# Kernel tuning notes

Hardware: AMD Instinct MI355X
Metric: run time of the kernel (lower is better)

## Reference

```python
import jax, jax.numpy as jnp
import numpy as np

N = 50000      # nodes
E = 400000     # edges per hop
IN = 256       # in_channels
H = 4          # heads
C = 64         # out_channels per head
NEG = 0.2      # leaky relu negative slope


def setup_inputs() -> dict:
    key = jax.random.key(0)
    ks = jax.random.split(key, 10)
    x = jax.random.normal(ks[0], (N, IN), dtype=jnp.float32)
    edge_index1 = jax.random.randint(ks[1], (2, E), 0, N, dtype=jnp.int32)
    edge_index2 = jax.random.randint(ks[2], (2, E), 0, N, dtype=jnp.int32)
    s = 0.05
    Wl0 = jax.random.normal(ks[3], (IN, H * C), dtype=jnp.float32) * s
    Wr0 = jax.random.normal(ks[4], (IN, H * C), dtype=jnp.float32) * s
    att0 = jax.random.normal(ks[5], (H, C), dtype=jnp.float32) * s
    Wl1 = jax.random.normal(ks[6], (IN, H * C), dtype=jnp.float32) * s
    Wr1 = jax.random.normal(ks[7], (IN, H * C), dtype=jnp.float32) * s
    att1 = jax.random.normal(ks[8], (H, C), dtype=jnp.float32) * s
    return {"x": x, "Wl0": Wl0, "Wr0": Wr0, "att0": att0,
            "Wl1": Wl1, "Wr1": Wr1, "att1": att1,
            "edge_index1": edge_index1, "edge_index2": edge_index2}


def _gatv2_hop(x, Wl, Wr, att, src, dst):
    """One GATv2Conv hop (bias=False, residual=False, eval-mode dropout, concat=False)."""
    n = x.shape[0]
    xl = (x @ Wl).reshape(n, H, C)   # source-side projection
    xr = (x @ Wr).reshape(n, H, C)   # target-side projection
    # edge-wise GATv2 score: a^T leaky_relu(x_l[j] + x_r[i])
    m = jax.nn.leaky_relu(xl[src] + xr[dst], NEG)            # [E, H, C]
    e = jnp.einsum('ehc,hc->eh', m, att)                     # [E, H]
    # segment softmax over incoming edges of each destination node
    e_max = jax.lax.stop_gradient(
        jax.ops.segment_max(e, dst, num_segments=n))         # [N, H]
    ex = jnp.exp(e - e_max[dst])
    denom = jax.ops.segment_sum(ex, dst, num_segments=n)     # [N, H]
    alpha = ex / (denom[dst] + 1e-16)                        # [E, H]
    msg = xl[src] * alpha[:, :, None]                        # [E, H, C]
    out = jax.ops.segment_sum(msg, dst, num_segments=n)      # [N, H, C]
    return out.mean(axis=1)                                  # concat=False -> mean heads


def reference(x, Wl0, Wr0, att0, Wl1, Wr1, att1, edge_index1, edge_index2):
    n = x.shape[0]
    # hop 0: add_self_loops=True
    loop = jnp.arange(n, dtype=edge_index1.dtype)
    src0 = jnp.concatenate([edge_index1[0], loop])
    dst0 = jnp.concatenate([edge_index1[1], loop])
    out = _gatv2_hop(x, Wl0, Wr0, att0, src0, dst0)
    # hop 1: no self loops, scaled by 1/(k+1) = 1/2
    out = out + _gatv2_hop(x, Wl1, Wr1, att1, edge_index2[0], edge_index2[1]) / 2.0
    return out
```

## Files before the change

### kernel.cpp

```cpp
#include <hip/hip_runtime.h>

typedef unsigned int uint;
typedef unsigned short ushort;

typedef __bf16 bf16x8 __attribute__((ext_vector_type(8)));
typedef float f32x4 __attribute__((ext_vector_type(4)));
typedef float f32x2 __attribute__((ext_vector_type(2)));

#define CAP 48
#define RSTR 136

__device__ __forceinline__ float bf2f(ushort u) {
    return __uint_as_float(((uint)u) << 16);
}
__device__ __forceinline__ ushort f2bf(float f) {
    uint u = __float_as_uint(f);
    u += 0x7fffu + ((u >> 16) & 1u);
    return (ushort)(u >> 16);
}
__device__ __forceinline__ void load_lds16(const ushort* g, ushort* l) {
    __builtin_amdgcn_global_load_lds(
        (const __attribute__((address_space(1))) void*)g,
        (__attribute__((address_space(3))) void*)l, 16, 0, 0);
}
__device__ __forceinline__ f32x2 up2(uint u) {
    f32x2 r;
    r.x = __uint_as_float(u << 16);
    r.y = __uint_as_float(u & 0xffff0000u);
    return r;
}

template<int CTRL>
__device__ __forceinline__ float dppadd(float p) {
    int t = __builtin_amdgcn_update_dpp(0, __float_as_int(p), CTRL, 0xf, 0xf, true);
    return p + __int_as_float(t);
}

__global__ __launch_bounds__(256) void prep_scatter(
    const float* __restrict__ X, ushort* __restrict__ Xb, int Nrows, int Mpad,
    const float* __restrict__ Wl0, const float* __restrict__ Wr0,
    const float* __restrict__ Wl1, const float* __restrict__ Wr1,
    ushort* __restrict__ Wt,
    const int* __restrict__ ei1, const int* __restrict__ ei2,
    int* __restrict__ cnt0, int* __restrict__ srcs0,
    int* __restrict__ cnt1, int* __restrict__ srcs1,
    int E1, int E2, int SB)
{
    int blk = blockIdx.x;
    if (blk < SB) {
        int e = blk * 256 + threadIdx.x;
        if (e < E1) {
            int d = ei1[E1 + e];
            int pos = atomicAdd(&cnt0[d], 1);
            if (pos < CAP) srcs0[(size_t)d * CAP + pos] = ei1[e];
        } else if (e < E1 + E2) {
            int e2 = e - E1;
            int d = ei2[E2 + e2];
            int pos = atomicAdd(&cnt1[d], 1);
            if (pos < CAP) srcs1[(size_t)d * CAP + pos] = ei2[e2];
        }
        return;
    }
    blk -= SB;
    const int BX = Mpad / 8;
    if (blk < BX) {
        int i = blk * 256 + threadIdx.x;
        int base = i * 8;
        int row = base >> 8;
        ushort o[8];
        if (row < Nrows) {
            float4 v0 = *(const float4*)(X + base);
            float4 v1 = *(const float4*)(X + base + 4);
            o[0] = f2bf(v0.x); o[1] = f2bf(v0.y); o[2] = f2bf(v0.z); o[3] = f2bf(v0.w);
            o[4] = f2bf(v1.x); o[5] = f2bf(v1.y); o[6] = f2bf(v1.z); o[7] = f2bf(v1.w);
        } else {
#pragma unroll
            for (int j = 0; j < 8; j++) o[j] = 0;
        }
        *(uint4*)(Xb + base) = *(const uint4*)o;
        return;
    }
    blk -= BX;
    int n = blk;
    int k = threadIdx.x;
    const float* W = (n < 256) ? Wl0 : (n < 512) ? Wr0 : (n < 768) ? Wl1 : Wr1;
    Wt[n * 256 + k] = f2bf(W[k * 256 + (n & 255)]);
}

__global__ __launch_bounds__(256, 4) void gemm_mfma(
    const ushort* __restrict__ Xb,
    const ushort* __restrict__ Wt,
    ushort* __restrict__ XP,
    int Nrows, int Pp, int nbshift)
{
    int b = blockIdx.x;
    int xcd = b & 7;
    int i = b >> 3;
    int p = xcd * Pp + (i >> nbshift);
    int j = i & ((1 << nbshift) - 1);
    const int m0 = p * 128;
    const int n0g = j * 128;

    __shared__ ushort SH[2 * 128 * 64];
    ushort* As = SH;
    ushort* Bs = SH + 128 * 64;

    const int tid = threadIdx.x;
    const int w = tid >> 6, l = tid & 63;
    const int wm = w & 1, wn = w >> 1;

    f32x4 acc[4][4];
#pragma unroll
    for (int ii = 0; ii < 4; ii++)
#pragma unroll
        for (int jj = 0; jj < 4; jj++) acc[ii][jj] = (f32x4)(0.f);

    const int fr = l & 15, fq = l >> 4;
    int a_off[2][4], b_off[2][4];
#pragma unroll
    for (int g = 0; g < 2; g++)
#pragma unroll
        for (int t = 0; t < 4; t++) {
            int c = g * 4 + fq;
            int rA = wm * 64 + t * 16 + fr;
            a_off[g][t] = (rA * 8 + ((c + rA) & 7)) * 8;
            int rB = wn * 64 + t * 16 + fr;
            b_off[g][t] = (rB * 8 + ((c + rB) & 7)) * 8;
        }

    for (int k0 = 0; k0 < 256; k0 += 64) {
        __syncthreads();
#pragma unroll
        for (int rnd = 0; rnd < 4; rnd++) {
            int slot = rnd * 256 + tid;
            int row = slot >> 3;
            int c = ((slot & 7) - row) & 7;
            load_lds16(Xb + (size_t)(m0 + row) * 256 + k0 + c * 8,
                       &As[(rnd * 256 + w * 64) * 8]);
            load_lds16(Wt + (size_t)(n0g + row) * 256 + k0 + c * 8,
                       &Bs[(rnd * 256 + w * 64) * 8]);
        }
        __syncthreads();

#pragma unroll
        for (int g = 0; g < 2; g++) {
            bf16x8 a[4], bfr[4];
#pragma unroll
            for (int t = 0; t < 4; t++) {
                a[t]   = *(const bf16x8*)(As + a_off[g][t]);
                bfr[t] = *(const bf16x8*)(Bs + b_off[g][t]);
            }
#pragma unroll
            for (int mi = 0; mi < 4; mi++)
#pragma unroll
                for (int ni = 0; ni < 4; ni++)
                    acc[mi][ni] = __builtin_amdgcn_mfma_f32_16x16x32_bf16(
                        a[mi], bfr[ni], acc[mi][ni], 0, 0, 0);
        }
    }

    ushort* OUT = XP + (size_t)(n0g >> 8) * ((size_t)Nrows * 256);
    const int colbase = n0g & 255;
    const int cb = wn * 64 + fr;
#pragma unroll
    for (int r = 0; r < 2; r++) {
        __syncthreads();
#pragma unroll
        for (int mm = 0; mm < 2; mm++) {
            int mi = 2 * r + mm;
            int brb = (wm * 32 + mm * 16 + fq * 4) * RSTR + cb;
#pragma unroll
            for (int reg = 0; reg < 4; reg++)
#pragma unroll
                for (int ni = 0; ni < 4; ni++)
                    SH[brb + reg * RSTR + ni * 16] = f2bf(acc[mi][ni][reg]);
        }
        __syncthreads();
        int br = tid >> 2;
        int grow = m0 + (br >> 5) * 64 + (2 * r + ((br >> 4) & 1)) * 16 + (br & 15);
        bool ok = (grow < Nrows);
        int cc = (tid & 3) * 8;
#pragma unroll
        for (int q = 0; q < 4; q++) {
            uint4 v = *(const uint4*)(SH + br * RSTR + cc + q * 32);
            if (ok) *(uint4*)(OUT + (size_t)grow * 256 + colbase + cc + q * 32) = v;
        }
    }
}

__device__ __forceinline__ uint4 pair_load(const ushort* __restrict__ XL, int sv,
                                           int e, int cp, uint hl, uint sub16)
{
    int eA = (e     < cp) ? e     : cp;
    int eB = (e + 1 < cp) ? e + 1 : cp;
    uint sA = (uint)__builtin_amdgcn_readlane(sv, eA) * 512u;
    uint sB = (uint)__builtin_amdgcn_readlane(sv, eB) * 512u;
    uint off = sA + hl * (sB - sA) + sub16;
    return *(const uint4*)((const char*)XL + off);
}

__device__ __forceinline__ void eaccp(uint4 raw, int deadB, uint hl,
    const f32x2* __restrict__ xr2, const f32x2* __restrict__ av2,
    f32x2* __restrict__ acc, float& den)
{
    f32x2 xv[4];
    xv[0] = up2(raw.x);
    xv[1] = up2(raw.y);
    xv[2] = up2(raw.z);
    xv[3] = up2(raw.w);
    f32x2 p2 = (f32x2)(0.f);
#pragma unroll
    for (int k = 0; k < 4; k++) {
        f32x2 t = xv[k] + xr2[k];
        f32x2 u = t * 0.2f;
        t.x = fmaxf(t.x, u.x);
        t.y = fmaxf(t.y, u.y);
        p2 += t * av2[k];
    }
    float p = p2.x + p2.y;
    p = dppadd<0xB1>(p);
    p = dppadd<0x4E>(p);
    p = dppadd<0x141>(p);
    float pe = __expf(p);
    if (deadB & (int)hl) pe = 0.f;
    den += pe;
#pragma unroll
    for (int k = 0; k < 4; k++) acc[k] += xv[k] * pe;
}

__device__ __forceinline__ void gat_hop(
    const ushort* __restrict__ XL, const ushort* __restrict__ XR,
    const float* __restrict__ att, const int* __restrict__ cnt,
    const int* __restrict__ srcs, int self, int d, int lane,
    uint hl, uint sub, uint sub16,
    f32x2* __restrict__ acc, float& den)
{
    uint4 xrr = *(const uint4*)((const char*)XR + (uint)d * 512u + sub16);
    f32x2 xr2[4];
    xr2[0] = up2(xrr.x);
    xr2[1] = up2(xrr.y);
    xr2[2] = up2(xrr.z);
    xr2[3] = up2(xrr.w);
    float4 a0 = *(const float4*)(att + sub * 8);
    float4 a1 = *(const float4*)(att + sub * 8 + 4);
    f32x2 av2[4];
    av2[0].x = a0.x; av2[0].y = a0.y;
    av2[1].x = a0.z; av2[1].y = a0.w;
    av2[2].x = a1.x; av2[2].y = a1.y;
    av2[3].x = a1.z; av2[3].y = a1.w;

#pragma unroll
    for (int k = 0; k < 4; k++) acc[k] = (f32x2)(0.f);
    den = 0.f;

    int m = __builtin_amdgcn_readfirstlane(cnt[d]);
    if (m > CAP) m = CAP;
    const int mt = m + self;
    if (mt <= 0) return;

    int idx = lane - self;
    int mm1 = (m > 0) ? (m - 1) : 0;
    int slot = idx < 0 ? 0 : (idx > mm1 ? mm1 : idx);
    int sv = srcs[(size_t)d * CAP + slot];
    if (self && lane == 0) sv = d;

    const int cp = mt - 1;
    uint4 pf0 = pair_load(XL, sv, 0, cp, hl, sub16);
    uint4 pf1 = pair_load(XL, sv, 2, cp, hl, sub16);
    for (int i = 0; i < mt; i += 4) {
        uint4 c0 = pf0, c1 = pf1;
        pf0 = pair_load(XL, sv, i + 4, cp, hl, sub16);
        pf1 = pair_load(XL, sv, i + 6, cp, hl, sub16);
        eaccp(c0, (i + 1 >= mt) ? 1 : 0, hl, xr2, av2, acc, den);
        if (i + 2 < mt)
            eaccp(c1, (i + 3 >= mt) ? 1 : 0, hl, xr2, av2, acc, den);
    }
}

__global__ __launch_bounds__(256) void gat_fused(
    const ushort* __restrict__ XL0, const ushort* __restrict__ XR0,
    const float* __restrict__ att0,
    const int* __restrict__ cnt0, const int* __restrict__ srcs0,
    int self0, float scale0,
    const ushort* __restrict__ XL1, const ushort* __restrict__ XR1,
    const float* __restrict__ att1,
    const int* __restrict__ cnt1, const int* __restrict__ srcs1,
    float scale1,
    const float* __restrict__ base, float* __restrict__ outp, int N)
{
    int d = blockIdx.x * 4 + (threadIdx.x >> 6);
    if (d >= N) return;
    int lane = threadIdx.x & 63;
    uint hl = (uint)(lane >> 5);
    uint sub = (uint)(lane & 31);
    uint sub16 = sub * 16u;

    f32x2 acc0[4];
    float den0;
    gat_hop(XL0, XR0, att0, cnt0, srcs0, self0, d, lane, hl, sub, sub16, acc0, den0);

    float v[8];
    den0 += __shfl_xor(den0, 32);
    float s0 = scale0 / (den0 + 1e-16f);
    if (cnt1) {
        f32x2 acc1[4];
        float den1;
        gat_hop(XL1, XR1, att1, cnt1, srcs1, 0, d, lane, hl, sub, sub16, acc1, den1);
        den1 += __shfl_xor(den1, 32);
        float s1 = scale1 / (den1 + 1e-16f);
#pragma unroll
        for (int k = 0; k < 4; k++) {
            v[2 * k]     = acc0[k].x * s0 + acc1[k].x * s1;
            v[2 * k + 1] = acc0[k].y * s0 + acc1[k].y * s1;
        }
    } else {
#pragma unroll
        for (int k = 0; k < 4; k++) {
            v[2 * k]     = acc0[k].x * s0;
            v[2 * k + 1] = acc0[k].y * s0;
        }
    }
#pragma unroll
    for (int j = 0; j < 8; j++) {
        v[j] += __shfl_xor(v[j], 8);
        v[j] += __shfl_xor(v[j], 16);
        v[j] += __shfl_xor(v[j], 32);
    }
    if (lane < 8) {
        float* dst = outp + (size_t)d * 64 + lane * 8;
        float4 w0 = {v[0], v[1], v[2], v[3]};
        float4 w1 = {v[4], v[5], v[6], v[7]};
        if (base) {
            float4 b0 = *(const float4*)(base + (size_t)d * 64 + lane * 8);
            float4 b1 = *(const float4*)(base + (size_t)d * 64 + lane * 8 + 4);
            w0.x += b0.x; w0.y += b0.y; w0.z += b0.z; w0.w += b0.w;
            w1.x += b1.x; w1.y += b1.y; w1.z += b1.z; w1.w += b1.w;
        }
        *(float4*)dst = w0;
        *(float4*)(dst + 4) = w1;
    }
}

extern "C" void kernel_launch(void* const* d_in, const int* in_sizes, int n_in,
                              void* d_out, int out_size, void* d_ws, size_t ws_size,
                              hipStream_t stream)
{
    const float* x    = (const float*)d_in[0];
    const float* Wl0  = (const float*)d_in[1];
    const float* Wr0  = (const float*)d_in[2];
    const float* att0 = (const float*)d_in[3];
    const float* Wl1  = (const float*)d_in[4];
    const float* Wr1  = (const float*)d_in[5];
    const float* att1 = (const float*)d_in[6];
    const int* ei1 = (const int*)d_in[7];
    const int* ei2 = (const int*)d_in[8];

    const int N  = in_sizes[0] / 256;
    const int E1 = in_sizes[7] / 2;
    const int E2 = in_sizes[8] / 2;
    const int Mpad = ((N + 1023) / 1024) * 1024;
    const int P  = Mpad / 128;
    const int Pp = P / 8;
    const size_t NB = (size_t)N * 256;

    char* ws = (char*)d_ws;
    size_t off = 0;
    ushort* Xb  = (ushort*)(ws + off); off += (size_t)Mpad * 256 * sizeof(ushort);
    ushort* Wt  = (ushort*)(ws + off); off += (size_t)1024 * 256 * sizeof(ushort);
    int* cnt0   = (int*)(ws + off);    off += (size_t)N * sizeof(int);
    int* cnt1   = (int*)(ws + off);    off += (size_t)N * sizeof(int);
    int* srcs0  = (int*)(ws + off);    off += (size_t)N * CAP * sizeof(int);
    int* srcs1  = (int*)(ws + off);    off += (size_t)N * CAP * sizeof(int);
    ushort* XP  = (ushort*)(ws + off);
    size_t need_mega = off + 4 * NB * sizeof(ushort);
    const bool mega = (ws_size >= need_mega);
    float* outf = (float*)d_out;

    hipMemsetAsync(cnt0, 0, 2 * (size_t)N * sizeof(int), stream);

    const int BX = Mpad / 8;
    const int SB = (E1 + E2 + 255) / 256;
    prep_scatter<<<SB + BX + 1024, 256, 0, stream>>>(
        x, Xb, N, Mpad, Wl0, Wr0, Wl1, Wr1, Wt,
        ei1, ei2, cnt0, srcs0, cnt1, srcs1, E1, E2, SB);

    int aggblk = (N + 3) / 4;
    if (mega) {
        gemm_mfma<<<P * 8, 256, 0, stream>>>(Xb, Wt, XP, N, Pp, 3);
        gat_fused<<<aggblk, 256, 0, stream>>>(
            XP, XP + NB, att0, cnt0, srcs0, 1, 0.25f,
            XP + 2 * NB, XP + 3 * NB, att1, cnt1, srcs1, 0.125f,
            nullptr, outf, N);
    } else {
        gemm_mfma<<<P * 4, 256, 0, stream>>>(Xb, Wt, XP, N, Pp, 2);
        gat_fused<<<aggblk, 256, 0, stream>>>(
            XP, XP + NB, att0, cnt0, srcs0, 1, 0.25f,
            nullptr, nullptr, nullptr, nullptr, nullptr, 0.f,
            nullptr, outf, N);
        gemm_mfma<<<P * 4, 256, 0, stream>>>(Xb, Wt + 512 * 256, XP, N, Pp, 2);
        gat_fused<<<aggblk, 256, 0, stream>>>(
            XP, XP + NB, att1, cnt1, srcs1, 0, 0.125f,
            nullptr, nullptr, nullptr, nullptr, nullptr, 0.f,
            outf, outf, N);
    }
}
```

Baseline: 256.7 us.

## Split the two GAT hops across separate wavefronts and combine partial results in LDS

The fused aggregation kernel used to process both hops serially inside one wavefront per destination node. It is replaced by a kernel that gives each (destination, hop) pair its own wavefront, two destinations per block, and sums the two hop results through shared memory before writing the output. The new kernel also issues up to eight pair loads up front to deepen memory-level parallelism on the neighbor gathers. The aim is to double the number of independent gather streams and cut per-wave latency. The costs are a block-level barrier, an LDS round trip, and more registers for the prefetch array, which could lower occupancy.

```diff
diff --git a/kernel.cpp b/kernel.cpp
--- a/kernel.cpp
+++ b/kernel.cpp
@@ -9,6 +9,7 @@
 
 #define CAP 48
 #define RSTR 136
+#define PFD 8
 
 __device__ __forceinline__ float bf2f(ushort u) {
     return __uint_as_float(((uint)u) << 16);
@@ -228,6 +229,107 @@
     for (int k = 0; k < 4; k++) acc[k] += xv[k] * pe;
 }
 
+__global__ __launch_bounds__(256) void gat_split(
+    const ushort* __restrict__ XP,
+    const float* __restrict__ att0, const float* __restrict__ att1,
+    const int* __restrict__ cnt0, const int* __restrict__ srcs0,
+    const int* __restrict__ cnt1, const int* __restrict__ srcs1,
+    float* __restrict__ outp, int N, size_t NB)
+{
+    __shared__ float part[4][64];
+    const int tid = threadIdx.x;
+    const int w = tid >> 6;
+    const int dst_i = w >> 1, hop = w & 1;
+    const int d = blockIdx.x * 2 + dst_i;
+    const int lane = tid & 63;
+    const uint hl = (uint)(lane >> 5);
+    const uint sub = (uint)(lane & 31);
+    const uint sub16 = sub * 16u;
+
+    if (d < N) {
+        const ushort* XL = hop ? XP + 2 * NB : XP;
+        const ushort* XR = XL + NB;
+        const float* att = hop ? att1 : att0;
+        const int* cnt   = hop ? cnt1 : cnt0;
+        const int* srcs  = hop ? srcs1 : srcs0;
+        const int self   = hop ? 0 : 1;
+        const float scale = hop ? 0.125f : 0.25f;
+
+        uint4 xrr = *(const uint4*)((const char*)XR + (uint)d * 512u + sub16);
+        int idxs = lane - self;
+        idxs = idxs < 0 ? 0 : (idxs > CAP - 1 ? CAP - 1 : idxs);
+        int sv = srcs[(size_t)d * CAP + idxs];
+        int m = __builtin_amdgcn_readfirstlane(cnt[d]);
+        float4 a0 = *(const float4*)(att + sub * 8);
+        float4 a1 = *(const float4*)(att + sub * 8 + 4);
+
+        f32x2 xr2[4];
+        xr2[0] = up2(xrr.x);
+        xr2[1] = up2(xrr.y);
+        xr2[2] = up2(xrr.z);
+        xr2[3] = up2(xrr.w);
+        f32x2 av2[4];
+        av2[0].x = a0.x; av2[0].y = a0.y;
+        av2[1].x = a0.z; av2[1].y = a0.w;
+        av2[2].x = a1.x; av2[2].y = a1.y;
+        av2[3].x = a1.z; av2[3].y = a1.w;
+
+        if (m > CAP) m = CAP;
+        const int mt = m + self;
+        if (self && lane == 0) sv = d;
+
+        f32x2 acc[4];
+#pragma unroll
+        for (int k = 0; k < 4; k++) acc[k] = (f32x2)(0.f);
+        float den = 0.f;
+
+        if (mt > 0) {
+            const int cp = mt - 1;
+            const int npair = (mt + 1) >> 1;
+            uint4 pf[PFD];
+#pragma unroll
+            for (int k = 0; k < PFD; k++)
+                if (k < npair) pf[k] = pair_load(XL, sv, 2 * k, cp, hl, sub16);
+#pragma unroll
+            for (int k = 0; k < PFD; k++)
+                if (k < npair)
+                    eaccp(pf[k], (2 * k + 1 >= mt) ? 1 : 0, hl, xr2, av2, acc, den);
+            for (int k = PFD; k < npair; k++) {
+                uint4 c = pair_load(XL, sv, 2 * k, cp, hl, sub16);
+                eaccp(c, (2 * k + 1 >= mt) ? 1 : 0, hl, xr2, av2, acc, den);
+            }
+        }
+
+        den += __shfl_xor(den, 32);
+        float s = scale / (den + 1e-16f);
+        float v[8];
+#pragma unroll
+        for (int k = 0; k < 4; k++) {
+            v[2 * k]     = acc[k].x * s;
+            v[2 * k + 1] = acc[k].y * s;
+        }
+#pragma unroll
+        for (int j = 0; j < 8; j++) {
+            v[j] += __shfl_xor(v[j], 8);
+            v[j] += __shfl_xor(v[j], 16);
+            v[j] += __shfl_xor(v[j], 32);
+        }
+        if (lane < 8) {
+            float4 w0 = {v[0], v[1], v[2], v[3]};
+            float4 w1 = {v[4], v[5], v[6], v[7]};
+            *(float4*)&part[w][lane * 8]     = w0;
+            *(float4*)&part[w][lane * 8 + 4] = w1;
+        }
+    }
+    __syncthreads();
+    if (tid < 128) {
+        int di = tid >> 6, ch = tid & 63;
+        int dd = blockIdx.x * 2 + di;
+        if (dd < N)
+            outp[(size_t)dd * 64 + ch] = part[di * 2][ch] + part[di * 2 + 1][ch];
+    }
+}
+
 __device__ __forceinline__ void gat_hop(
     const ushort* __restrict__ XL, const ushort* __restrict__ XR,
     const float* __restrict__ att, const int* __restrict__ cnt,
@@ -282,10 +384,6 @@
     const float* __restrict__ att0,
     const int* __restrict__ cnt0, const int* __restrict__ srcs0,
     int self0, float scale0,
-    const ushort* __restrict__ XL1, const ushort* __restrict__ XR1,
-    const float* __restrict__ att1,
-    const int* __restrict__ cnt1, const int* __restrict__ srcs1,
-    float scale1,
     const float* __restrict__ base, float* __restrict__ outp, int N)
 {
     int d = blockIdx.x * 4 + (threadIdx.x >> 6);
@@ -302,23 +400,10 @@
     float v[8];
     den0 += __shfl_xor(den0, 32);
     float s0 = scale0 / (den0 + 1e-16f);
-    if (cnt1) {
-        f32x2 acc1[4];
-        float den1;
-        gat_hop(XL1, XR1, att1, cnt1, srcs1, 0, d, lane, hl, sub, sub16, acc1, den1);
-        den1 += __shfl_xor(den1, 32);
-        float s1 = scale1 / (den1 + 1e-16f);
-#pragma unroll
-        for (int k = 0; k < 4; k++) {
-            v[2 * k]     = acc0[k].x * s0 + acc1[k].x * s1;
-            v[2 * k + 1] = acc0[k].y * s0 + acc1[k].y * s1;
-        }
-    } else {
-#pragma unroll
-        for (int k = 0; k < 4; k++) {
-            v[2 * k]     = acc0[k].x * s0;
-            v[2 * k + 1] = acc0[k].y * s0;
-        }
+#pragma unroll
+    for (int k = 0; k < 4; k++) {
+        v[2 * k]     = acc0[k].x * s0;
+        v[2 * k + 1] = acc0[k].y * s0;
     }
 #pragma unroll
     for (int j = 0; j < 8; j++) {
@@ -384,23 +469,19 @@
         x, Xb, N, Mpad, Wl0, Wr0, Wl1, Wr1, Wt,
         ei1, ei2, cnt0, srcs0, cnt1, srcs1, E1, E2, SB);
 
-    int aggblk = (N + 3) / 4;
     if (mega) {
         gemm_mfma<<<P * 8, 256, 0, stream>>>(Xb, Wt, XP, N, Pp, 3);
-        gat_fused<<<aggblk, 256, 0, stream>>>(
-            XP, XP + NB, att0, cnt0, srcs0, 1, 0.25f,
-            XP + 2 * NB, XP + 3 * NB, att1, cnt1, srcs1, 0.125f,
-            nullptr, outf, N);
+        gat_split<<<(N + 1) / 2, 256, 0, stream>>>(
+            XP, att0, att1, cnt0, srcs0, cnt1, srcs1, outf, N, NB);
     } else {
+        int aggblk = (N + 3) / 4;
         gemm_mfma<<<P * 4, 256, 0, stream>>>(Xb, Wt, XP, N, Pp, 2);
         gat_fused<<<aggblk, 256, 0, stream>>>(
             XP, XP + NB, att0, cnt0, srcs0, 1, 0.25f,
-            nullptr, nullptr, nullptr, nullptr, nullptr, 0.f,
             nullptr, outf, N);
         gemm_mfma<<<P * 4, 256, 0, stream>>>(Xb, Wt + 512 * 256, XP, N, Pp, 2);
         gat_fused<<<aggblk, 256, 0, stream>>>(
             XP, XP + NB, att1, cnt1, srcs1, 0, 0.125f,
-            nullptr, nullptr, nullptr, nullptr, nullptr, 0.f,
             outf, outf, N);
     }
 }
```

After: 267.2 us. 1.04x slower.

## Fuse fp32-to-bf16 conversion of X into GEMM A-tile loading

Applied to the files above, without the earlier changes.

Drops the separate pass in the prep kernel that converts X to a bf16 buffer. The GEMM now reads fp32 X directly, packs it to bf16 with v_cvt_pk_bf16_f32, and stores the A tile to LDS with ordinary stores. The B tile still uses direct global-to-LDS loads. This removes a full write and re-read of the bf16 copy of X, but each GEMM block now reads twice the bytes for A. In the mega path every row tile is reloaded by 8 column blocks, so A is read as fp32 several times, and the A-tile path adds register pressure. The leaky-relu max also becomes a vector elementwise max.

```diff
diff --git a/kernel.cpp b/kernel.cpp
--- a/kernel.cpp
+++ b/kernel.cpp
@@ -10,9 +10,6 @@
 #define CAP 48
 #define RSTR 136
 
-__device__ __forceinline__ float bf2f(ushort u) {
-    return __uint_as_float(((uint)u) << 16);
-}
 __device__ __forceinline__ ushort f2bf(float f) {
     uint u = __float_as_uint(f);
     u += 0x7fffu + ((u >> 16) & 1u);
@@ -22,6 +19,11 @@
     __builtin_amdgcn_global_load_lds(
         (const __attribute__((address_space(1))) void*)g,
         (__attribute__((address_space(3))) void*)l, 16, 0, 0);
+}
+__device__ __forceinline__ uint cvtpk(float lo, float hi) {
+    uint r;
+    asm("v_cvt_pk_bf16_f32 %0, %1, %2" : "=v"(r) : "v"(lo), "v"(hi));
+    return r;
 }
 __device__ __forceinline__ f32x2 up2(uint u) {
     f32x2 r;
@@ -37,7 +39,6 @@
 }
 
 __global__ __launch_bounds__(256) void prep_scatter(
-    const float* __restrict__ X, ushort* __restrict__ Xb, int Nrows, int Mpad,
     const float* __restrict__ Wl0, const float* __restrict__ Wr0,
     const float* __restrict__ Wl1, const float* __restrict__ Wr1,
     ushort* __restrict__ Wt,
@@ -62,25 +63,6 @@
         return;
     }
     blk -= SB;
-    const int BX = Mpad / 8;
-    if (blk < BX) {
-        int i = blk * 256 + threadIdx.x;
-        int base = i * 8;
-        int row = base >> 8;
-        ushort o[8];
-        if (row < Nrows) {
-            float4 v0 = *(const float4*)(X + base);
-            float4 v1 = *(const float4*)(X + base + 4);
-            o[0] = f2bf(v0.x); o[1] = f2bf(v0.y); o[2] = f2bf(v0.z); o[3] = f2bf(v0.w);
-            o[4] = f2bf(v1.x); o[5] = f2bf(v1.y); o[6] = f2bf(v1.z); o[7] = f2bf(v1.w);
-        } else {
-#pragma unroll
-            for (int j = 0; j < 8; j++) o[j] = 0;
-        }
-        *(uint4*)(Xb + base) = *(const uint4*)o;
-        return;
-    }
-    blk -= BX;
     int n = blk;
     int k = threadIdx.x;
     const float* W = (n < 256) ? Wl0 : (n < 512) ? Wr0 : (n < 768) ? Wl1 : Wr1;
@@ -88,7 +70,7 @@
 }
 
 __global__ __launch_bounds__(256, 4) void gemm_mfma(
-    const ushort* __restrict__ Xb,
+    const float* __restrict__ X,
     const ushort* __restrict__ Wt,
     ushort* __restrict__ XP,
     int Nrows, int Pp, int nbshift)
@@ -128,17 +110,40 @@
             b_off[g][t] = (rB * 8 + ((c + rB) & 7)) * 8;
         }
 
+    int srow[4], schunk[4];
+#pragma unroll
+    for (int rnd = 0; rnd < 4; rnd++) {
+        int slot = rnd * 256 + tid;
+        srow[rnd] = slot >> 3;
+        schunk[rnd] = ((slot & 7) - srow[rnd]) & 7;
+    }
+
     for (int k0 = 0; k0 < 256; k0 += 64) {
         __syncthreads();
 #pragma unroll
+        for (int rnd = 0; rnd < 4; rnd++)
+            load_lds16(Wt + (size_t)(n0g + srow[rnd]) * 256 + k0 + schunk[rnd] * 8,
+                       &Bs[(rnd * 256 + w * 64) * 8]);
+        float4 va[4], vb[4];
+#pragma unroll
         for (int rnd = 0; rnd < 4; rnd++) {
-            int slot = rnd * 256 + tid;
-            int row = slot >> 3;
-            int c = ((slot & 7) - row) & 7;
-            load_lds16(Xb + (size_t)(m0 + row) * 256 + k0 + c * 8,
-                       &As[(rnd * 256 + w * 64) * 8]);
-            load_lds16(Wt + (size_t)(n0g + row) * 256 + k0 + c * 8,
-                       &Bs[(rnd * 256 + w * 64) * 8]);
+            int grow = m0 + srow[rnd];
+            va[rnd] = (float4){0.f, 0.f, 0.f, 0.f};
+            vb[rnd] = (float4){0.f, 0.f, 0.f, 0.f};
+            if (grow < Nrows) {
+                const float* src = X + (size_t)grow * 256 + k0 + schunk[rnd] * 8;
+                va[rnd] = *(const float4*)src;
+                vb[rnd] = *(const float4*)(src + 4);
+            }
+        }
+#pragma unroll
+        for (int rnd = 0; rnd < 4; rnd++) {
+            uint4 pk;
+            pk.x = cvtpk(va[rnd].x, va[rnd].y);
+            pk.y = cvtpk(va[rnd].z, va[rnd].w);
+            pk.z = cvtpk(vb[rnd].x, vb[rnd].y);
+            pk.w = cvtpk(vb[rnd].z, vb[rnd].w);
+            *(uint4*)(As + (rnd * 256 + tid) * 8) = pk;
         }
         __syncthreads();
 
@@ -213,8 +218,7 @@
     for (int k = 0; k < 4; k++) {
         f32x2 t = xv[k] + xr2[k];
         f32x2 u = t * 0.2f;
-        t.x = fmaxf(t.x, u.x);
-        t.y = fmaxf(t.y, u.y);
+        t = __builtin_elementwise_max(t, u);
         p2 += t * av2[k];
     }
     float p = p2.x + p2.y;
@@ -365,7 +369,6 @@
 
     char* ws = (char*)d_ws;
     size_t off = 0;
-    ushort* Xb  = (ushort*)(ws + off); off += (size_t)Mpad * 256 * sizeof(ushort);
     ushort* Wt  = (ushort*)(ws + off); off += (size_t)1024 * 256 * sizeof(ushort);
     int* cnt0   = (int*)(ws + off);    off += (size_t)N * sizeof(int);
     int* cnt1   = (int*)(ws + off);    off += (size_t)N * sizeof(int);
@@ -378,26 +381,25 @@
 
     hipMemsetAsync(cnt0, 0, 2 * (size_t)N * sizeof(int), stream);
 
-    const int BX = Mpad / 8;
     const int SB = (E1 + E2 + 255) / 256;
-    prep_scatter<<<SB + BX + 1024, 256, 0, stream>>>(
-        x, Xb, N, Mpad, Wl0, Wr0, Wl1, Wr1, Wt,
+    prep_scatter<<<SB + 1024, 256, 0, stream>>>(
+        Wl0, Wr0, Wl1, Wr1, Wt,
         ei1, ei2, cnt0, srcs0, cnt1, srcs1, E1, E2, SB);
 
     int aggblk = (N + 3) / 4;
     if (mega) {
-        gemm_mfma<<<P * 8, 256, 0, stream>>>(Xb, Wt, XP, N, Pp, 3);
+        gemm_mfma<<<P * 8, 256, 0, stream>>>(x, Wt, XP, N, Pp, 3);
         gat_fused<<<aggblk, 256, 0, stream>>>(
             XP, XP + NB, att0, cnt0, srcs0, 1, 0.25f,
             XP + 2 * NB, XP + 3 * NB, att1, cnt1, srcs1, 0.125f,
             nullptr, outf, N);
     } else {
-        gemm_mfma<<<P * 4, 256, 0, stream>>>(Xb, Wt, XP, N, Pp, 2);
+        gemm_mfma<<<P * 4, 256, 0, stream>>>(x, Wt, XP, N, Pp, 2);
         gat_fused<<<aggblk, 256, 0, stream>>>(
             XP, XP + NB, att0, cnt0, srcs0, 1, 0.25f,
             nullptr, nullptr, nullptr, nullptr, nullptr, 0.f,
             nullptr, outf, N);
-        gemm_mfma<<<P * 4, 256, 0, stream>>>(Xb, Wt + 512 * 256, XP, N, Pp, 2);
+        gemm_mfma<<<P * 4, 256, 0, stream>>>(x, Wt + 512 * 256, XP, N, Pp, 2);
         gat_fused<<<aggblk, 256, 0, stream>>>(
             XP, XP + NB, att1, cnt1, srcs1, 0, 0.125f,
             nullptr, nullptr, nullptr, nullptr, nullptr, 0.f,
```

New measurement: 321.8 us. 25.4% more time.
